# Kernel tuning notes

Measured on AMD Instinct MI355X. Metric: run time of the kernel, lower is better.

Reference implementation:

```python
import jax, jax.numpy as jnp
import numpy as np

N_NODES = 100000
N_EDGES = 800000
IN_DIM, HID_DIM, OUT_DIM = 128, 256, 128


def setup_inputs() -> dict:
    key = jax.random.key(0)
    k1, k2, k3, k4, k5 = jax.random.split(key, 5)
    x = jax.random.normal(k1, (N_NODES, IN_DIM), dtype=jnp.float32)
    edge_index = jax.random.randint(k2, (2, N_EDGES), 0, N_NODES, dtype=jnp.int64)
    edge_weight = jax.random.uniform(k3, (N_EDGES,), dtype=jnp.float32)
    W1 = jax.random.normal(k4, (IN_DIM, HID_DIM), dtype=jnp.float32) * 0.02
    b1 = jnp.zeros((HID_DIM,), dtype=jnp.float32)
    W2 = jax.random.normal(k5, (HID_DIM, OUT_DIM), dtype=jnp.float32) * 0.02
    b2 = jnp.zeros((OUT_DIM,), dtype=jnp.float32)
    return {"x": x, "edge_index": edge_index, "edge_weight": edge_weight,
            "W1": W1, "b1": b1, "W2": W2, "b2": b2}


def reference(x, edge_index, edge_weight, W1, b1, W2, b2):
    # GCNConv (normalize=True, add_self_loops=False), two layers with ReLU.
    # Dropout is identity at inference.
    row = edge_index[0]  # source nodes (E,)
    col = edge_index[1]  # target nodes (E,)
    n = x.shape[0]

    # Symmetric normalization: deg at target, norm = d^-1/2[row]*w*d^-1/2[col]
    deg = jax.ops.segment_sum(edge_weight, col, num_segments=n)  # (N,)
    dis = jnp.where(deg > 0, jax.lax.rsqrt(deg), 0.0)
    norm = dis[row] * edge_weight * dis[col]  # (E,)

    def gcn_conv(h, W, b):
        h = h @ W                                   # (N, F_out)
        msg = h[row] * norm[:, None]                # (E, F_out) gather+scale
        agg = jax.ops.segment_sum(msg, col, num_segments=n)  # scatter-add
        return agg + b

    h = jax.nn.relu(gcn_conv(x.astype(jnp.float32), W1, b1))
    return gcn_conv(h, W2, b2)
```

## Files before the change

kernel.cpp:

```cpp
#include <hip/hip_runtime.h>
#include <hip/hip_bf16.h>
#include <cstdint>
#include <cstddef>

#define N_NODES 100000
#define N_EDGES 800000
#define IN_DIM 128
#define HID_DIM 256
#define OUT_DIM 128

typedef __attribute__((ext_vector_type(8))) short bf16x8;
typedef __attribute__((ext_vector_type(4))) float f32x4;

__device__ __forceinline__ unsigned short f32_to_bf16(float f) {
    __hip_bfloat16 b = __float2bfloat16(f);
    return *reinterpret_cast<unsigned short*>(&b);
}
__device__ __forceinline__ float bf16_lo(uint32_t u) {
    uint32_t v = u << 16; return *reinterpret_cast<float*>(&v);
}
__device__ __forceinline__ float bf16_hi(uint32_t u) {
    uint32_t v = u & 0xffff0000u; return *reinterpret_cast<float*>(&v);
}

__global__ void rank_hist_kernel(const int* __restrict__ ei,
                                 const float* __restrict__ ew,
                                 int* __restrict__ cnt,
                                 float* __restrict__ deg,
                                 int* __restrict__ rank) {
    int e = blockIdx.x * 256 + threadIdx.x;
    if (e >= N_EDGES) return;
    int c = ei[N_EDGES + e];
    rank[e] = atomicAdd(&cnt[c], 1);
    atomicAdd(&deg[c], ew[e]);
}

__global__ void scan1_kernel(const int* __restrict__ in, int* __restrict__ out,
                             int* __restrict__ bsums, int n) {
    __shared__ int tmp[256];
    int t = threadIdx.x;
    int i = blockIdx.x * 256 + t;
    int v = (i < n) ? in[i] : 0;
    tmp[t] = v;
    __syncthreads();
    for (int off = 1; off < 256; off <<= 1) {
        int u = (t >= off) ? tmp[t - off] : 0;
        __syncthreads();
        tmp[t] += u;
        __syncthreads();
    }
    if (i < n) out[i] = tmp[t] - v;
    if (t == 255) bsums[blockIdx.x] = tmp[255];
}

__global__ void scan2_kernel(int* __restrict__ bsums, int nb) {
    __shared__ int tmp[512];
    int t = threadIdx.x;
    int v = (t < nb) ? bsums[t] : 0;
    tmp[t] = v;
    __syncthreads();
    for (int off = 1; off < 512; off <<= 1) {
        int u = (t >= off) ? tmp[t - off] : 0;
        __syncthreads();
        tmp[t] += u;
        __syncthreads();
    }
    if (t < nb) bsums[t] = tmp[t] - v;
}

__global__ void scan3_kernel(int* __restrict__ rowp, const int* __restrict__ bsums,
                             const float* __restrict__ deg, float* __restrict__ dis,
                             int n, int total) {
    int i = blockIdx.x * 256 + threadIdx.x;
    if (i == 0) rowp[n] = total;
    if (i >= n) return;
    rowp[i] += bsums[blockIdx.x];
    float d = deg[i];
    dis[i] = d > 0.f ? rsqrtf(d) : 0.f;
}

__global__ void place_kernel(const int* __restrict__ ei,
                             const float* __restrict__ ew,
                             const int* __restrict__ rank,
                             const int* __restrict__ rowp,
                             const float* __restrict__ dis,
                             int2* __restrict__ pairs) {
    int e = blockIdx.x * 256 + threadIdx.x;
    if (e >= N_EDGES) return;
    int s = ei[e];
    int c = ei[N_EDGES + e];
    int pos = rowp[c] + rank[e];
    float wn = ew[e] * dis[s] * dis[c];
    pairs[pos] = make_int2(s, __float_as_int(wn));
}

__global__ void prep_kernel(const float* __restrict__ x, uint32_t* __restrict__ xb,
                            const float* __restrict__ W1, unsigned short* __restrict__ W1F,
                            const float* __restrict__ W2, unsigned short* __restrict__ W2F) {
    int b = blockIdx.x;
    if (b < 12500) {
        int i = b * 256 + threadIdx.x;
        float4 v = ((const float4*)x)[i];
        uint32_t lo = (uint32_t)f32_to_bf16(v.x) | ((uint32_t)f32_to_bf16(v.y) << 16);
        uint32_t hi = (uint32_t)f32_to_bf16(v.z) | ((uint32_t)f32_to_bf16(v.w) << 16);
        ((uint2*)xb)[i] = make_uint2(lo, hi);
    } else if (b < 12628) {
        int idx = (b - 12500) * 256 + threadIdx.x;
        int j = idx & 7, lane = (idx >> 3) & 63;
        int nt = (idx >> 9) & 3, ks = (idx >> 11) & 3;
        int wc = (idx >> 13) & 1, nh = (idx >> 14) & 1;
        int fr = lane & 15, fq = lane >> 4;
        int row = nh * 128 + wc * 64 + nt * 16 + fr;
        int kk = ks * 32 + fq * 8 + j;
        W1F[idx] = f32_to_bf16(W1[kk * HID_DIM + row]);
    } else {
        int idx = (b - 12628) * 256 + threadIdx.x;
        int j = idx & 7, lane = (idx >> 3) & 63;
        int nt = (idx >> 9) & 3, ks = (idx >> 11) & 3;
        int wc = (idx >> 13) & 1, nh = (idx >> 14) & 1;
        int fr = lane & 15, fq = lane >> 4;
        int n = wc * 64 + nt * 16 + fr;
        int kk = nh * 128 + ks * 32 + fq * 8 + j;
        W2F[idx] = f32_to_bf16(W2[kk * OUT_DIM + n]);
    }
}

__device__ __forceinline__ void acc_edge(float w, uint4 u, float* a) {
    a[0] += w * bf16_lo(u.x); a[1] += w * bf16_hi(u.x);
    a[2] += w * bf16_lo(u.y); a[3] += w * bf16_hi(u.y);
    a[4] += w * bf16_lo(u.z); a[5] += w * bf16_hi(u.z);
    a[6] += w * bf16_lo(u.w); a[7] += w * bf16_hi(u.w);
}

template <bool OUT_BF16>
__global__ void aggregate_kernel(const uint4* __restrict__ feat,
                                 const int* __restrict__ rowp,
                                 const int2* __restrict__ pairs,
                                 void* __restrict__ out_v,
                                 const float* __restrict__ bias) {
    int gtid = blockIdx.x * blockDim.x + threadIdx.x;
    int node = gtid >> 4;
    int lane = threadIdx.x & 15;
    if (node >= N_NODES) return;
    int beg = rowp[node], end = rowp[node + 1];
    float a[8] = {};

    int j = beg;
    for (; j + 4 <= end; j += 4) {
        int2 p[4]; uint4 u[4];
        #pragma unroll
        for (int q = 0; q < 4; ++q) p[q] = pairs[j + q];
        #pragma unroll
        for (int q = 0; q < 4; ++q) u[q] = feat[(size_t)p[q].x * 16 + lane];
        #pragma unroll
        for (int q = 0; q < 4; ++q) acc_edge(__int_as_float(p[q].y), u[q], a);
    }
    if (j + 2 <= end) {
        int2 p0 = pairs[j], p1 = pairs[j + 1];
        uint4 u0 = feat[(size_t)p0.x * 16 + lane];
        uint4 u1 = feat[(size_t)p1.x * 16 + lane];
        acc_edge(__int_as_float(p0.y), u0, a);
        acc_edge(__int_as_float(p1.y), u1, a);
        j += 2;
    }
    if (j < end) {
        int2 p0 = pairs[j];
        uint4 u0 = feat[(size_t)p0.x * 16 + lane];
        acc_edge(__int_as_float(p0.y), u0, a);
    }
    if (bias) {
        float4 b0 = ((const float4*)bias)[lane * 2];
        float4 b1 = ((const float4*)bias)[lane * 2 + 1];
        a[0] += b0.x; a[1] += b0.y; a[2] += b0.z; a[3] += b0.w;
        a[4] += b1.x; a[5] += b1.y; a[6] += b1.z; a[7] += b1.w;
    }
    if (OUT_BF16) {
        uint4 o;
        o.x = (uint32_t)f32_to_bf16(a[0]) | ((uint32_t)f32_to_bf16(a[1]) << 16);
        o.y = (uint32_t)f32_to_bf16(a[2]) | ((uint32_t)f32_to_bf16(a[3]) << 16);
        o.z = (uint32_t)f32_to_bf16(a[4]) | ((uint32_t)f32_to_bf16(a[5]) << 16);
        o.w = (uint32_t)f32_to_bf16(a[6]) | ((uint32_t)f32_to_bf16(a[7]) << 16);
        ((uint4*)out_v)[(size_t)node * 16 + lane] = o;
    } else {
        ((float4*)out_v)[(size_t)node * 32 + lane * 2] =
            make_float4(a[0], a[1], a[2], a[3]);
        ((float4*)out_v)[(size_t)node * 32 + lane * 2 + 1] =
            make_float4(a[4], a[5], a[6], a[7]);
    }
}

__global__ __launch_bounds__(256, 2) void gemm_fused_kernel(
    const unsigned short* __restrict__ A,
    const unsigned short* __restrict__ W1F,
    const float* __restrict__ b1,
    const unsigned short* __restrict__ W2F,
    unsigned short* __restrict__ T,
    int M) {
    __shared__ unsigned short As[128 * 128];
    __shared__ unsigned short Hs[128 * 136];
    int tid = threadIdx.x;
    int wave = tid >> 6, lane = tid & 63;
    int m0 = blockIdx.x * 128;
    int wr = (wave & 1) * 64;
    int wcid = wave >> 1;
    int wc = wcid * 64;
    int fr = lane & 15, fq = lane >> 4;

    #pragma unroll
    for (int i = 0; i < 8; ++i) {
        int cbase = (i * 4 + wave) * 64;
        int c = cbase + lane;
        int m = c >> 4, cl = c & 15;
        int qg = ((cl & 7) ^ (m & 7)) | (cl & 8);
        int gm = m0 + m; if (gm >= M) gm = M - 1;
        const unsigned short* ga = A + (size_t)gm * 128 + qg * 8;
        __builtin_amdgcn_global_load_lds(
            (const __attribute__((address_space(1))) void*)ga,
            (__attribute__((address_space(3))) void*)(As + (size_t)cbase * 8),
            16, 0, 0);
    }
    __syncthreads();

    bf16x8 af[4][4];
    #pragma unroll
    for (int ks = 0; ks < 4; ++ks) {
        int q = ks * 4 + fq;
        int cl = ((q & 7) ^ (fr & 7)) | (q & 8);
        #pragma unroll
        for (int mt = 0; mt < 4; ++mt)
            af[ks][mt] = *(const bf16x8*)(As + (wr + mt * 16 + fr) * 128 + cl * 8);
    }

    const bf16x8* w1p = (const bf16x8*)W1F;
    const bf16x8* w2p = (const bf16x8*)W2F;

    f32x4 acc_t[4][4] = {};
    #pragma unroll
    for (int nh = 0; nh < 2; ++nh) {
        int wbase = (nh * 2 + wcid) * 16 * 64;
        f32x4 acc_h[4][4] = {};
        #pragma unroll
        for (int ks = 0; ks < 4; ++ks) {
            bf16x8 wf[4];
            #pragma unroll
            for (int nt = 0; nt < 4; ++nt)
                wf[nt] = w1p[wbase + (ks * 4 + nt) * 64 + lane];
            #pragma unroll
            for (int mt = 0; mt < 4; ++mt)
                #pragma unroll
                for (int nt = 0; nt < 4; ++nt)
                    acc_h[mt][nt] = __builtin_amdgcn_mfma_f32_16x16x32_bf16(
                        af[ks][mt], wf[nt], acc_h[mt][nt], 0, 0, 0);
        }
        float bv[4];
        #pragma unroll
        for (int nt = 0; nt < 4; ++nt) bv[nt] = b1[nh * 128 + wc + nt * 16 + fr];
        __syncthreads();
        #pragma unroll
        for (int mt = 0; mt < 4; ++mt)
            #pragma unroll
            for (int r = 0; r < 4; ++r) {
                int row = wr + mt * 16 + fq * 4 + r;
                #pragma unroll
                for (int nt = 0; nt < 4; ++nt) {
                    float v = fmaxf(acc_h[mt][nt][r] + bv[nt], 0.f);
                    Hs[row * 136 + wc + nt * 16 + fr] = f32_to_bf16(v);
                }
            }
        __syncthreads();
        #pragma unroll
        for (int ks = 0; ks < 4; ++ks) {
            bf16x8 wf[4], hf[4];
            #pragma unroll
            for (int nt = 0; nt < 4; ++nt)
                wf[nt] = w2p[wbase + (ks * 4 + nt) * 64 + lane];
            #pragma unroll
            for (int mt = 0; mt < 4; ++mt)
                hf[mt] = *(const bf16x8*)(Hs + (wr + mt * 16 + fr) * 136 + ks * 32 + fq * 8);
            #pragma unroll
            for (int mt = 0; mt < 4; ++mt)
                #pragma unroll
                for (int nt = 0; nt < 4; ++nt)
                    acc_t[mt][nt] = __builtin_amdgcn_mfma_f32_16x16x32_bf16(
                        hf[mt], wf[nt], acc_t[mt][nt], 0, 0, 0);
        }
    }

    #pragma unroll
    for (int mt = 0; mt < 4; ++mt)
        #pragma unroll
        for (int r = 0; r < 4; ++r) {
            int row = m0 + wr + mt * 16 + fq * 4 + r;
            if (row >= M) continue;
            #pragma unroll
            for (int nt = 0; nt < 4; ++nt)
                T[(size_t)row * 128 + wc + nt * 16 + fr] = f32_to_bf16(acc_t[mt][nt][r]);
        }
}

extern "C" void kernel_launch(void* const* d_in, const int* in_sizes, int n_in,
                              void* d_out, int out_size, void* d_ws, size_t ws_size,
                              hipStream_t stream) {
    const float* x  = (const float*)d_in[0];
    const int*   ei = (const int*)d_in[1];
    const float* ew = (const float*)d_in[2];
    const float* W1 = (const float*)d_in[3];
    const float* b1 = (const float*)d_in[4];
    const float* W2 = (const float*)d_in[5];
    const float* b2 = (const float*)d_in[6];
    float* out = (float*)d_out;

    char* ws = (char*)d_ws;
    size_t off = 0;
    auto alloc = [&](size_t bytes) -> void* {
        void* p = ws + off;
        off = (off + bytes + 255) & ~(size_t)255;
        return p;
    };
    int*   cnt   = (int*)  alloc((size_t)N_NODES * 8);
    float* deg   = (float*)(cnt + N_NODES);
    float* dis   = (float*)alloc((size_t)N_NODES * 4);
    int*   rowp  = (int*)  alloc((size_t)(N_NODES + 1) * 4);
    int*   bsums = (int*)  alloc(512 * 4);
    int*   rank  = (int*)  alloc((size_t)N_EDGES * 4);
    int2*  pairs = (int2*) alloc((size_t)N_EDGES * 8);
    uint32_t* xb = (uint32_t*)alloc((size_t)N_NODES * IN_DIM * 2);
    unsigned short* W1F = (unsigned short*)alloc((size_t)IN_DIM * HID_DIM * 2);
    unsigned short* W2F = (unsigned short*)alloc((size_t)HID_DIM * OUT_DIM * 2);
    unsigned short* A1  = (unsigned short*)alloc((size_t)N_NODES * IN_DIM * 2);
    unsigned short* t   = (unsigned short*)alloc((size_t)N_NODES * OUT_DIM * 2);

    hipMemsetAsync(cnt, 0, (size_t)N_NODES * 8, stream);

    int ne_blocks = (N_EDGES + 255) / 256;
    int nn_blocks = (N_NODES + 255) / 256;

    rank_hist_kernel<<<ne_blocks, 256, 0, stream>>>(ei, ew, cnt, deg, rank);
    scan1_kernel<<<nn_blocks, 256, 0, stream>>>(cnt, rowp, bsums, N_NODES);
    scan2_kernel<<<1, 512, 0, stream>>>(bsums, nn_blocks);
    scan3_kernel<<<nn_blocks, 256, 0, stream>>>(rowp, bsums, deg, dis, N_NODES, N_EDGES);
    place_kernel<<<ne_blocks, 256, 0, stream>>>(ei, ew, rank, rowp, dis, pairs);
    prep_kernel<<<12756, 256, 0, stream>>>(x, xb, W1, W1F, W2, W2F);

    int agg_blocks = (N_NODES * 16) / 256;

    aggregate_kernel<true><<<agg_blocks, 256, 0, stream>>>(
        (const uint4*)xb, rowp, pairs, A1, nullptr);

    gemm_fused_kernel<<<(N_NODES + 127) / 128, 256, 0, stream>>>(
        A1, W1F, b1, W2F, t, N_NODES);

    aggregate_kernel<false><<<agg_blocks, 256, 0, stream>>>(
        (const uint4*)t, rowp, pairs, out, b2);
}
```

Baseline: 309.8 us.

## Merge histogram with bf16 prep and compute degree from CSR instead of float atomics

New measurement: 281.8 us. 9.0% less time.

```diff
diff --git a/kernel.cpp b/kernel.cpp
--- a/kernel.cpp
+++ b/kernel.cpp
@@ -23,16 +23,50 @@
     uint32_t v = u & 0xffff0000u; return *reinterpret_cast<float*>(&v);
 }
 
-__global__ void rank_hist_kernel(const int* __restrict__ ei,
-                                 const float* __restrict__ ew,
+#define HIST_BLOCKS 3125
+#define XB_BLOCKS 12500
+
+__global__ void hist_prep_kernel(const int* __restrict__ ei,
                                  int* __restrict__ cnt,
-                                 float* __restrict__ deg,
-                                 int* __restrict__ rank) {
-    int e = blockIdx.x * 256 + threadIdx.x;
-    if (e >= N_EDGES) return;
-    int c = ei[N_EDGES + e];
-    rank[e] = atomicAdd(&cnt[c], 1);
-    atomicAdd(&deg[c], ew[e]);
+                                 int* __restrict__ rank,
+                                 const float* __restrict__ x,
+                                 uint32_t* __restrict__ xb,
+                                 const float* __restrict__ W1,
+                                 unsigned short* __restrict__ W1F,
+                                 const float* __restrict__ W2,
+                                 unsigned short* __restrict__ W2F) {
+    int b = blockIdx.x;
+    if (b < HIST_BLOCKS) {
+        int e = b * 256 + threadIdx.x;
+        rank[e] = atomicAdd(&cnt[ei[N_EDGES + e]], 1);
+        return;
+    }
+    b -= HIST_BLOCKS;
+    if (b < XB_BLOCKS) {
+        int i = b * 256 + threadIdx.x;
+        float4 v = ((const float4*)x)[i];
+        uint32_t lo = (uint32_t)f32_to_bf16(v.x) | ((uint32_t)f32_to_bf16(v.y) << 16);
+        uint32_t hi = (uint32_t)f32_to_bf16(v.z) | ((uint32_t)f32_to_bf16(v.w) << 16);
+        ((uint2*)xb)[i] = make_uint2(lo, hi);
+    } else if (b < XB_BLOCKS + 128) {
+        int idx = (b - XB_BLOCKS) * 256 + threadIdx.x;
+        int j = idx & 7, lane = (idx >> 3) & 63;
+        int nt = (idx >> 9) & 3, ks = (idx >> 11) & 3;
+        int wc = (idx >> 13) & 1, nh = (idx >> 14) & 1;
+        int fr = lane & 15, fq = lane >> 4;
+        int row = nh * 128 + wc * 64 + nt * 16 + fr;
+        int kk = ks * 32 + fq * 8 + j;
+        W1F[idx] = f32_to_bf16(W1[kk * HID_DIM + row]);
+    } else {
+        int idx = (b - XB_BLOCKS - 128) * 256 + threadIdx.x;
+        int j = idx & 7, lane = (idx >> 3) & 63;
+        int nt = (idx >> 9) & 3, ks = (idx >> 11) & 3;
+        int wc = (idx >> 13) & 1, nh = (idx >> 14) & 1;
+        int fr = lane & 15, fq = lane >> 4;
+        int n = wc * 64 + nt * 16 + fr;
+        int kk = nh * 128 + ks * 32 + fq * 8 + j;
+        W2F[idx] = f32_to_bf16(W2[kk * OUT_DIM + n]);
+    }
 }
 
 __global__ void scan1_kernel(const int* __restrict__ in, int* __restrict__ out,
@@ -69,59 +103,47 @@
 }
 
 __global__ void scan3_kernel(int* __restrict__ rowp, const int* __restrict__ bsums,
-                             const float* __restrict__ deg, float* __restrict__ dis,
                              int n, int total) {
     int i = blockIdx.x * 256 + threadIdx.x;
     if (i == 0) rowp[n] = total;
     if (i >= n) return;
     rowp[i] += bsums[blockIdx.x];
-    float d = deg[i];
-    dis[i] = d > 0.f ? rsqrtf(d) : 0.f;
 }
 
 __global__ void place_kernel(const int* __restrict__ ei,
                              const float* __restrict__ ew,
                              const int* __restrict__ rank,
                              const int* __restrict__ rowp,
-                             const float* __restrict__ dis,
                              int2* __restrict__ pairs) {
     int e = blockIdx.x * 256 + threadIdx.x;
     if (e >= N_EDGES) return;
-    int s = ei[e];
     int c = ei[N_EDGES + e];
     int pos = rowp[c] + rank[e];
-    float wn = ew[e] * dis[s] * dis[c];
-    pairs[pos] = make_int2(s, __float_as_int(wn));
-}
-
-__global__ void prep_kernel(const float* __restrict__ x, uint32_t* __restrict__ xb,
-                            const float* __restrict__ W1, unsigned short* __restrict__ W1F,
-                            const float* __restrict__ W2, unsigned short* __restrict__ W2F) {
-    int b = blockIdx.x;
-    if (b < 12500) {
-        int i = b * 256 + threadIdx.x;
-        float4 v = ((const float4*)x)[i];
-        uint32_t lo = (uint32_t)f32_to_bf16(v.x) | ((uint32_t)f32_to_bf16(v.y) << 16);
-        uint32_t hi = (uint32_t)f32_to_bf16(v.z) | ((uint32_t)f32_to_bf16(v.w) << 16);
-        ((uint2*)xb)[i] = make_uint2(lo, hi);
-    } else if (b < 12628) {
-        int idx = (b - 12500) * 256 + threadIdx.x;
-        int j = idx & 7, lane = (idx >> 3) & 63;
-        int nt = (idx >> 9) & 3, ks = (idx >> 11) & 3;
-        int wc = (idx >> 13) & 1, nh = (idx >> 14) & 1;
-        int fr = lane & 15, fq = lane >> 4;
-        int row = nh * 128 + wc * 64 + nt * 16 + fr;
-        int kk = ks * 32 + fq * 8 + j;
-        W1F[idx] = f32_to_bf16(W1[kk * HID_DIM + row]);
-    } else {
-        int idx = (b - 12628) * 256 + threadIdx.x;
-        int j = idx & 7, lane = (idx >> 3) & 63;
-        int nt = (idx >> 9) & 3, ks = (idx >> 11) & 3;
-        int wc = (idx >> 13) & 1, nh = (idx >> 14) & 1;
-        int fr = lane & 15, fq = lane >> 4;
-        int n = wc * 64 + nt * 16 + fr;
-        int kk = nh * 128 + ks * 32 + fq * 8 + j;
-        W2F[idx] = f32_to_bf16(W2[kk * OUT_DIM + n]);
+    pairs[pos] = make_int2(ei[e], __float_as_int(ew[e]));
+}
+
+__global__ void deg_dis_kernel(const int* __restrict__ rowp,
+                               const int2* __restrict__ pairs,
+                               float* __restrict__ dis) {
+    int v = blockIdx.x * 256 + threadIdx.x;
+    if (v >= N_NODES) return;
+    int b = rowp[v], e = rowp[v + 1];
+    float d = 0.f;
+    for (int j = b; j < e; ++j) d += __int_as_float(pairs[j].y);
+    dis[v] = d > 0.f ? rsqrtf(d) : 0.f;
+}
+
+__global__ void normalize_kernel(const int* __restrict__ rowp,
+                                 int2* __restrict__ pairs,
+                                 const float* __restrict__ dis) {
+    int v = blockIdx.x * 256 + threadIdx.x;
+    if (v >= N_NODES) return;
+    float dv = dis[v];
+    int b = rowp[v], e = rowp[v + 1];
+    for (int j = b; j < e; ++j) {
+        int2 p = pairs[j];
+        p.y = __float_as_int(__int_as_float(p.y) * dis[p.x] * dv);
+        pairs[j] = p;
     }
 }
 
@@ -317,8 +339,7 @@
         off = (off + bytes + 255) & ~(size_t)255;
         return p;
     };
-    int*   cnt   = (int*)  alloc((size_t)N_NODES * 8);
-    float* deg   = (float*)(cnt + N_NODES);
+    int*   cnt   = (int*)  alloc((size_t)N_NODES * 4);
     float* dis   = (float*)alloc((size_t)N_NODES * 4);
     int*   rowp  = (int*)  alloc((size_t)(N_NODES + 1) * 4);
     int*   bsums = (int*)  alloc(512 * 4);
@@ -330,17 +351,20 @@
     unsigned short* A1  = (unsigned short*)alloc((size_t)N_NODES * IN_DIM * 2);
     unsigned short* t   = (unsigned short*)alloc((size_t)N_NODES * OUT_DIM * 2);
 
-    hipMemsetAsync(cnt, 0, (size_t)N_NODES * 8, stream);
-
+    hipMemsetAsync(cnt, 0, (size_t)N_NODES * 4, stream);
+
+    int nn_blocks = (N_NODES + 255) / 256;
     int ne_blocks = (N_EDGES + 255) / 256;
-    int nn_blocks = (N_NODES + 255) / 256;
-
-    rank_hist_kernel<<<ne_blocks, 256, 0, stream>>>(ei, ew, cnt, deg, rank);
+
+    hist_prep_kernel<<<HIST_BLOCKS + XB_BLOCKS + 256, 256, 0, stream>>>(
+        ei, cnt, rank, x, xb, W1, W1F, W2, W2F);
+
     scan1_kernel<<<nn_blocks, 256, 0, stream>>>(cnt, rowp, bsums, N_NODES);
     scan2_kernel<<<1, 512, 0, stream>>>(bsums, nn_blocks);
-    scan3_kernel<<<nn_blocks, 256, 0, stream>>>(rowp, bsums, deg, dis, N_NODES, N_EDGES);
-    place_kernel<<<ne_blocks, 256, 0, stream>>>(ei, ew, rank, rowp, dis, pairs);
-    prep_kernel<<<12756, 256, 0, stream>>>(x, xb, W1, W1F, W2, W2F);
+    scan3_kernel<<<nn_blocks, 256, 0, stream>>>(rowp, bsums, N_NODES, N_EDGES);
+    place_kernel<<<ne_blocks, 256, 0, stream>>>(ei, ew, rank, rowp, pairs);
+    deg_dis_kernel<<<nn_blocks, 256, 0, stream>>>(rowp, pairs, dis);
+    normalize_kernel<<<nn_blocks, 256, 0, stream>>>(rowp, pairs, dis);
 
     int agg_blocks = (N_NODES * 16) / 256;
 
```
